# Kernel tuning notes

Measured on AMD Instinct MI355X. Metric: run time of the kernel, lower is better.

Reference implementation:

```python
import jax, jax.numpy as jnp
import numpy as np

B, M, D = 8, 4096, 512   # batch, seq_len, dim
E, P, H = 64, 1, 2048    # num_experts, slots_per_expert, expert hidden (4*dim)


def _l2norm(v, axis):
    # matches torch.nn.functional.normalize(p=2, eps=1e-12)
    n = jnp.linalg.norm(v, axis=axis, keepdims=True)
    return v / jnp.maximum(n, 1e-12)


def setup_inputs() -> dict:
    key = jax.random.key(0)
    ks = jax.random.split(key, 5)
    return {
        "x": jax.random.normal(ks[0], (B, M, D), dtype=jnp.float32),
        # phi init: normal(0, 1/sqrt(dim)) as in the module
        "phi": jax.random.normal(ks[1], (D, E, P), dtype=jnp.float32) * (1.0 / np.sqrt(D)),
        "scale": jnp.ones((1,), dtype=jnp.float32),
        # stacked expert MLP params (dim -> 4*dim -> dim, exact GELU)
        "w1": jax.random.normal(ks[2], (E, D, H), dtype=jnp.float32) * (1.0 / np.sqrt(D)),
        "b1": jnp.zeros((E, H), dtype=jnp.float32),
        "w2": jax.random.normal(ks[3], (E, H, D), dtype=jnp.float32) * (1.0 / np.sqrt(H)),
        "b2": jnp.zeros((E, D), dtype=jnp.float32),
    }


def reference(x, phi, scale, w1, b1, w2, b2):
    # Soft-MoE (algorithm 1, arXiv:2308.00951) with normalize=True
    xn = _l2norm(x, -1)                       # [B, M, D]
    phin = scale * _l2norm(phi, 0)            # [D, E, P]
    logits = jnp.einsum('bmd,dnp->bmnp', xn, phin)           # [B, M, E, P]
    d = jax.nn.softmax(logits, axis=1)                        # softmax over tokens m
    b_, m_, e_, p_ = logits.shape
    c = jax.nn.softmax(logits.reshape(b_, m_, e_ * p_), axis=-1).reshape(b_, m_, e_, p_)  # softmax over (n, p)
    xs = jnp.einsum('bmd,bmnp->bnpd', xn, d)                  # dispatch: [B, E, P, D]
    # per-expert MLP applied as grouped GEMM over expert axis n
    h = jax.nn.gelu(jnp.einsum('bnpd,ndh->bnph', xs, w1) + b1[None, :, None, :],
                    approximate=False)
    ys = jnp.einsum('bnph,nhd->bnpd', h, w2) + b2[None, :, None, :]  # [B, E, P, D]
    y = jnp.einsum('bnpd,bmnp->bmd', ys, c)                   # combine: [B, M, D]
    return y
```

## Files before the change

kernel.cpp:

```cpp
#include <hip/hip_runtime.h>
#include <hip/hip_bf16.h>
#include <math.h>


namespace {
constexpr int B = 8, M = 4096, D = 512, E = 64, H = 2048;
constexpr int NSD = 32;
constexpr int NK2 = 16;

constexpr size_t OFF_PHT  = 0;
constexpr size_t OFF_XNB  = OFF_PHT  + (size_t)D * E / 2;
constexpr size_t OFF_LOGB = OFF_XNB  + (size_t)B * M * D / 2;
constexpr size_t OFF_PMAX = OFF_LOGB + (size_t)B * M * E / 2;
constexpr size_t OFF_PSUM = OFF_PMAX + (size_t)B * NSD * E;
constexpr size_t OFF_XSP  = OFF_PSUM + (size_t)B * NSD * E;
constexpr size_t OFF_XSF  = OFF_XSP  + (size_t)NSD * B * E * D / 2;
constexpr size_t OFF_YSP  = OFF_XSF  + (size_t)E * D * B;
constexpr size_t OFF_YST  = OFF_YSP  + (size_t)NK2 * E * D * B / 2;
constexpr size_t WS_FLOATS = OFF_YST + (size_t)B * D * E / 2;
}

typedef __attribute__((ext_vector_type(8))) short short8v;
typedef __attribute__((ext_vector_type(4))) float f32x4;

static __device__ inline unsigned short f2bf(float f) {
  __hip_bfloat16 h = __float2bfloat16(f);
  return *reinterpret_cast<unsigned short*>(&h);
}
static __device__ inline float bf2f(unsigned short u) {
  unsigned int x = ((unsigned int)u) << 16;
  return __uint_as_float(x);
}
static __device__ inline short8v ld4w(const unsigned int* p, int a) {
  union { unsigned int u[4]; short8v v; } x;
  x.u[0] = p[a]; x.u[1] = p[a + 1]; x.u[2] = p[a + 2]; x.u[3] = p[a + 3];
  return x.v;
}

__global__ __launch_bounds__(256) void k_phinorm(const float* __restrict__ phi,
                                                 const float* __restrict__ scale,
                                                 unsigned short* __restrict__ phT) {
  int e = blockIdx.x;
  int t = threadIdx.x;
  float v0 = phi[(size_t)t * E + e];
  float v1 = phi[(size_t)(t + 256) * E + e];
  __shared__ float red[256];
  red[t] = v0 * v0 + v1 * v1;
  __syncthreads();
  for (int s = 128; s; s >>= 1) {
    if (t < s) red[t] += red[t + s];
    __syncthreads();
  }
  float inv = scale[0] / fmaxf(sqrtf(red[0]), 1e-12f);
  phT[(size_t)e * D + t]       = f2bf(v0 * inv);
  phT[(size_t)e * D + t + 256] = f2bf(v1 * inv);
}

__global__ __launch_bounds__(256) void k_logdis(const float* __restrict__ x,
                                                const unsigned short* __restrict__ phT,
                                                unsigned short* __restrict__ xnb,
                                                unsigned short* __restrict__ logitsb,
                                                float* __restrict__ pmax,
                                                float* __restrict__ psum,
                                                unsigned short* __restrict__ xs_part) {
  __shared__ __align__(16) unsigned char pool[80896];
  unsigned short* phs = (unsigned short*)pool;
  unsigned short* xA  = (unsigned short*)(pool + 66560);
  unsigned int* weT = (unsigned int*)pool;
  unsigned int* xnT = (unsigned int*)(pool + 16640);
  unsigned short* rp = (unsigned short*)(pool + 49920);
  __shared__ float invs[128];
  __shared__ float smax[4][64];
  __shared__ float bmax[64];
  int t = threadIdx.x;
  int lane = t & 63, w = t >> 6;
  int blk = blockIdx.x;
  int b = blk >> 5, ms = blk & 31;
  int rowbase = blk * 128;
  {
    int e = t >> 2, q0 = (t & 3) * 16;
#pragma unroll
    for (int q = 0; q < 16; q++)
      *(short8v*)&phs[e * 520 + (q0 + q) * 8] =
          *(const short8v*)&phT[(size_t)e * D + (q0 + q) * 8];
  }
  int srow = t >> 1;
  int kb = (t & 1) * 16;
  float ss = 0.f;
  f32x4 acc[2][4];
#pragma unroll
  for (int i = 0; i < 2; i++)
#pragma unroll
    for (int j = 0; j < 4; j++) acc[i][j] = (f32x4)(0.f);
  int kg = lane >> 4;
  int l15 = lane & 15;
  for (int ks = 0; ks < 16; ks++) {
    __syncthreads();
    const float4* xp = (const float4*)(x + (size_t)(rowbase + srow) * D + ks * 32 + kb);
#pragma unroll
    for (int q = 0; q < 4; q++) {
      float4 v = xp[q];
      ss += v.x * v.x + v.y * v.y + v.z * v.z + v.w * v.w;
      ushort4 u;
      u.x = f2bf(v.x); u.y = f2bf(v.y); u.z = f2bf(v.z); u.w = f2bf(v.w);
      *(ushort4*)&xA[srow * 56 + kb + q * 4] = u;
    }
    __syncthreads();
    {
      uint4 x0 = *(uint4*)&xA[srow * 56 + kb];
      uint4 x1 = *(uint4*)&xA[srow * 56 + kb + 8];
      size_t go = (size_t)(rowbase + srow) * D + ks * 32 + kb;
      *(uint4*)&xnb[go]     = x0;
      *(uint4*)&xnb[go + 8] = x1;
    }
    short8v a0 = *(short8v*)&xA[(w * 32 + l15) * 56 + kg * 8];
    short8v a1 = *(short8v*)&xA[(w * 32 + 16 + l15) * 56 + kg * 8];
    short8v b0 = *(short8v*)&phs[(l15)      * 520 + ks * 32 + kg * 8];
    short8v b1 = *(short8v*)&phs[(16 + l15) * 520 + ks * 32 + kg * 8];
    short8v b2 = *(short8v*)&phs[(32 + l15) * 520 + ks * 32 + kg * 8];
    short8v b3 = *(short8v*)&phs[(48 + l15) * 520 + ks * 32 + kg * 8];
    acc[0][0] = __builtin_amdgcn_mfma_f32_16x16x32_bf16(a0, b0, acc[0][0], 0, 0, 0);
    acc[0][1] = __builtin_amdgcn_mfma_f32_16x16x32_bf16(a0, b1, acc[0][1], 0, 0, 0);
    acc[0][2] = __builtin_amdgcn_mfma_f32_16x16x32_bf16(a0, b2, acc[0][2], 0, 0, 0);
    acc[0][3] = __builtin_amdgcn_mfma_f32_16x16x32_bf16(a0, b3, acc[0][3], 0, 0, 0);
    acc[1][0] = __builtin_amdgcn_mfma_f32_16x16x32_bf16(a1, b0, acc[1][0], 0, 0, 0);
    acc[1][1] = __builtin_amdgcn_mfma_f32_16x16x32_bf16(a1, b1, acc[1][1], 0, 0, 0);
    acc[1][2] = __builtin_amdgcn_mfma_f32_16x16x32_bf16(a1, b2, acc[1][2], 0, 0, 0);
    acc[1][3] = __builtin_amdgcn_mfma_f32_16x16x32_bf16(a1, b3, acc[1][3], 0, 0, 0);
  }
  ss += __shfl_xor(ss, 1, 64);
  float iv = 1.0f / fmaxf(sqrtf(ss), 1e-12f);
  if ((t & 1) == 0) invs[srow] = iv;
  __syncthreads();
  int rsub = kg * 4;
  float lm[4] = {-1e30f, -1e30f, -1e30f, -1e30f};
#pragma unroll
  for (int fi = 0; fi < 2; fi++)
#pragma unroll
    for (int r = 0; r < 4; r++) {
      int row = w * 32 + fi * 16 + rsub + r;
      float ivr = invs[row];
#pragma unroll
      for (int eg = 0; eg < 4; eg++) {
        float v = acc[fi][eg][r] * ivr;
        logitsb[(size_t)(rowbase + row) * E + eg * 16 + l15] = f2bf(v);
        lm[eg] = fmaxf(lm[eg], v);
      }
    }
#pragma unroll
  for (int eg = 0; eg < 4; eg++) {
    lm[eg] = fmaxf(lm[eg], __shfl_xor(lm[eg], 16, 64));
    lm[eg] = fmaxf(lm[eg], __shfl_xor(lm[eg], 32, 64));
  }
  if (lane < 16)
#pragma unroll
    for (int eg = 0; eg < 4; eg++) smax[w][eg * 16 + lane] = lm[eg];
  __syncthreads();
  if (t < 64)
    bmax[t] = fmaxf(fmaxf(smax[0][t], smax[1][t]), fmaxf(smax[2][t], smax[3][t]));
  __syncthreads();
  float ps[4] = {0.f, 0.f, 0.f, 0.f};
#pragma unroll
  for (int fi = 0; fi < 2; fi++)
#pragma unroll
    for (int r2 = 0; r2 < 2; r2++) {
      int rowA = w * 32 + fi * 16 + rsub + 2 * r2;
      float iv0 = invs[rowA], iv1 = invs[rowA + 1];
#pragma unroll
      for (int eg = 0; eg < 4; eg++) {
        float bm = bmax[eg * 16 + l15];
        float p0 = __expf(acc[fi][eg][2 * r2]     * iv0 - bm);
        float p1 = __expf(acc[fi][eg][2 * r2 + 1] * iv1 - bm);
        ps[eg] += p0 + p1;
        weT[(eg * 16 + l15) * 65 + (w * 16 + fi * 8 + (rsub >> 1) + r2)] =
            (unsigned int)f2bf(p0 * iv0) | ((unsigned int)f2bf(p1 * iv1) << 16);
      }
    }
#pragma unroll
  for (int eg = 0; eg < 4; eg++) {
    ps[eg] += __shfl_xor(ps[eg], 16, 64);
    ps[eg] += __shfl_xor(ps[eg], 32, 64);
  }
  __syncthreads();
  if (lane < 16)
#pragma unroll
    for (int eg = 0; eg < 4; eg++) smax[w][eg * 16 + lane] = ps[eg];
  __syncthreads();
  if (t < 64) {
    pmax[(size_t)blk * 64 + t] = bmax[t];
    psum[(size_t)blk * 64 + t] =
        smax[0][t] + smax[1][t] + smax[2][t] + smax[3][t];
  }
  unsigned short* outp = xs_part + ((size_t)ms * B + b) * E * D;
  for (int dc = 0; dc < 4; dc++) {
    __syncthreads();
#pragma unroll
    for (int i = 0; i < 16; i++) {
      int flat = i * 256 + t;
      int mp = flat >> 6, d2 = flat & 63;
      size_t rbase = (size_t)(rowbase + 2 * mp) * D + dc * 128 + d2 * 2;
      unsigned int ua = *(const unsigned int*)&xnb[rbase];
      unsigned int ub = *(const unsigned int*)&xnb[rbase + D];
      xnT[(2 * d2 + 0) * 65 + mp] = (ua & 0xffffu) | ((ub & 0xffffu) << 16);
      xnT[(2 * d2 + 1) * 65 + mp] = (ua >> 16) | (ub & 0xffff0000u);
    }
    __syncthreads();
    f32x4 ac3[4][2];
#pragma unroll
    for (int i = 0; i < 4; i++) { ac3[i][0] = (f32x4)(0.f); ac3[i][1] = (f32x4)(0.f); }
#pragma unroll
    for (int ks2 = 0; ks2 < 4; ks2++) {
      short8v afr[4];
#pragma unroll
      for (int et = 0; et < 4; et++)
        afr[et] = ld4w(weT, (et * 16 + l15) * 65 + ks2 * 16 + kg * 4);
#pragma unroll
      for (int dtl = 0; dtl < 2; dtl++) {
        short8v bfr = ld4w(xnT, (w * 32 + dtl * 16 + l15) * 65 + ks2 * 16 + kg * 4);
#pragma unroll
        for (int et = 0; et < 4; et++)
          ac3[et][dtl] = __builtin_amdgcn_mfma_f32_16x16x32_bf16(afr[et], bfr, ac3[et][dtl], 0, 0, 0);
      }
    }
#pragma unroll
    for (int et = 0; et < 4; et++)
#pragma unroll
      for (int dtl = 0; dtl < 2; dtl++)
#pragma unroll
        for (int r = 0; r < 4; r++) {
          int e = et * 16 + rsub + r;
          int d = w * 32 + dtl * 16 + l15;
          rp[e * 136 + d] = f2bf(ac3[et][dtl][r]);
        }
    __syncthreads();
    {
      int g = t >> 4, dch = t & 15;
#pragma unroll
      for (int pp = 0; pp < 4; pp++) {
        int el = pp * 16 + g;
        uint4 v = *(uint4*)&rp[el * 136 + dch * 8];
        *(uint4*)(outp + (size_t)el * D + dc * 128 + dch * 8) = v;
      }
    }
  }
}

__global__ __launch_bounds__(256) void k_xsred(const unsigned short* __restrict__ xs_part,
                                               const float* __restrict__ pmax,
                                               const float* __restrict__ psum,
                                               float* __restrict__ xs_f) {
  int blk = blockIdx.x;
  int b = blk >> 6, e = blk & 63;
  int t = threadIdx.x;
  float gm = -1e30f;
  for (int s = 0; s < NSD; s++)
    gm = fmaxf(gm, pmax[((size_t)(b * NSD + s)) * 64 + e]);
  float gs = 0.f;
  for (int s = 0; s < NSD; s++)
    gs += psum[((size_t)(b * NSD + s)) * 64 + e] *
          __expf(pmax[((size_t)(b * NSD + s)) * 64 + e] - gm);
  float inv = 1.0f / gs;
  size_t base = (((size_t)b * E + e) * D) / 2 + t;
  size_t slab = ((size_t)B * E * D) / 2;
  float a0 = 0.f, a1 = 0.f;
  const unsigned int* pp = (const unsigned int*)xs_part;
  for (int s = 0; s < NSD; s++) {
    float f = __expf(pmax[((size_t)(b * NSD + s)) * 64 + e] - gm);
    unsigned int v = pp[(size_t)s * slab + base];
    a0 += f * bf2f((unsigned short)(v & 0xffff));
    a1 += f * bf2f((unsigned short)(v >> 16));
  }
  int d = t * 2;
  xs_f[((size_t)e * D + d) * B + b]     = a0 * inv;
  xs_f[((size_t)e * D + d + 1) * B + b] = a1 * inv;
}

__global__ __launch_bounds__(256) void k_mlp(const float* __restrict__ w1,
                                             const float* __restrict__ b1,
                                             const float* __restrict__ w2,
                                             const float* __restrict__ xs_f,
                                             unsigned short* __restrict__ ys_part) {
  __shared__ float xsm[512 * 8];
  __shared__ float rbuf[4224];
  __shared__ float hsm[128 * 8];
  int blk = blockIdx.x;
  int e = blk >> 4, s = blk & 15;
  int t = threadIdx.x;
  const float4* xsrc = (const float4*)(xs_f + (size_t)e * D * B);
#pragma unroll
  for (int k = 0; k < 4; k++) ((float4*)xsm)[t + 256 * k] = xsrc[t + 256 * k];
  __syncthreads();
  int oct = t >> 5, jt = t & 31;
  int j0 = s * 128 + jt * 4;
  {
    const float* wp = w1 + ((size_t)e * D + oct * 64) * H + j0;
    const float* xb = xsm + oct * 64 * 8;
    float acc[4][8];
#pragma unroll
    for (int i = 0; i < 4; i++)
#pragma unroll
      for (int j = 0; j < 8; j++) acc[i][j] = 0.f;
#pragma unroll 8
    for (int d = 0; d < 64; d++) {
      float4 w = *(const float4*)(wp + (size_t)d * H);
      float x8[8];
      *(float4*)&x8[0] = *(float4*)&xb[d * 8];
      *(float4*)&x8[4] = *(float4*)&xb[d * 8 + 4];
#pragma unroll
      for (int bb = 0; bb < 8; bb++) {
        acc[0][bb] += w.x * x8[bb]; acc[1][bb] += w.y * x8[bb];
        acc[2][bb] += w.z * x8[bb]; acc[3][bb] += w.w * x8[bb];
      }
    }
    if (oct >= 4) {
      float* rb = &rbuf[((oct - 4) * 32 + jt) * 33];
#pragma unroll
      for (int i = 0; i < 4; i++) {
        *(float4*)(rb + i * 8)     = *(float4*)&acc[i][0];
        *(float4*)(rb + i * 8 + 4) = *(float4*)&acc[i][4];
      }
    }
    __syncthreads();
    if (oct < 4) {
      const float* rb = &rbuf[(oct * 32 + jt) * 33];
#pragma unroll
      for (int i = 0; i < 4; i++)
#pragma unroll
        for (int j = 0; j < 8; j++) acc[i][j] += rb[i * 8 + j];
    }
    __syncthreads();
    if (oct == 2 || oct == 3) {
      float* rb = &rbuf[((oct - 2) * 32 + jt) * 33];
#pragma unroll
      for (int i = 0; i < 4; i++) {
        *(float4*)(rb + i * 8)     = *(float4*)&acc[i][0];
        *(float4*)(rb + i * 8 + 4) = *(float4*)&acc[i][4];
      }
    }
    __syncthreads();
    if (oct < 2) {
      const float* rb = &rbuf[(oct * 32 + jt) * 33];
#pragma unroll
      for (int i = 0; i < 4; i++)
#pragma unroll
        for (int j = 0; j < 8; j++) acc[i][j] += rb[i * 8 + j];
    }
    __syncthreads();
    if (oct == 1) {
      float* rb = &rbuf[jt * 33];
#pragma unroll
      for (int i = 0; i < 4; i++) {
        *(float4*)(rb + i * 8)     = *(float4*)&acc[i][0];
        *(float4*)(rb + i * 8 + 4) = *(float4*)&acc[i][4];
      }
    }
    __syncthreads();
    if (oct == 0) {
      const float* rb = &rbuf[jt * 33];
      float4 bi = *(const float4*)(b1 + (size_t)e * H + j0);
      float bv[4] = {bi.x, bi.y, bi.z, bi.w};
#pragma unroll
      for (int i = 0; i < 4; i++)
#pragma unroll
        for (int j = 0; j < 8; j++) {
          float v = acc[i][j] + rb[i * 8 + j] + bv[i];
          hsm[(jt * 4 + i) * 8 + j] = 0.5f * v * (1.0f + erff(v * 0.70710678118654752f));
        }
    }
  }
  __syncthreads();
  {
    int kk = t >> 7, dq = t & 127;
    int d0 = dq * 4;
    const float* wp = w2 + ((size_t)e * H + s * 128 + kk * 64) * D + d0;
    const float* hb = hsm + kk * 64 * 8;
    float acc[4][8];
#pragma unroll
    for (int i = 0; i < 4; i++)
#pragma unroll
      for (int j = 0; j < 8; j++) acc[i][j] = 0.f;
#pragma unroll 8
    for (int k = 0; k < 64; k++) {
      float4 w = *(const float4*)(wp + (size_t)k * D);
      float h8[8];
      *(float4*)&h8[0] = *(float4*)&hb[k * 8];
      *(float4*)&h8[4] = *(float4*)&hb[k * 8 + 4];
#pragma unroll
      for (int bb = 0; bb < 8; bb++) {
        acc[0][bb] += w.x * h8[bb]; acc[1][bb] += w.y * h8[bb];
        acc[2][bb] += w.z * h8[bb]; acc[3][bb] += w.w * h8[bb];
      }
    }
    if (kk) {
#pragma unroll
      for (int i = 0; i < 4; i++) {
        *(float4*)&rbuf[dq * 32 + i * 8]     = *(float4*)&acc[i][0];
        *(float4*)&rbuf[dq * 32 + i * 8 + 4] = *(float4*)&acc[i][4];
      }
    }
    __syncthreads();
    if (!kk) {
      unsigned short* op = ys_part + (((size_t)s * E + e) * D + d0) * B;
#pragma unroll
      for (int i = 0; i < 4; i++) {
        unsigned short us[8];
#pragma unroll
        for (int j = 0; j < 8; j++)
          us[j] = f2bf(acc[i][j] + rbuf[dq * 32 + i * 8 + j]);
        *(uint4*)(op + (size_t)i * 8) = *(uint4*)us;
      }
    }
  }
}

__global__ __launch_bounds__(256) void k_ysred(const unsigned short* __restrict__ ys_part,
                                               const float* __restrict__ b2,
                                               unsigned short* __restrict__ ysT) {
  int e = blockIdx.x >> 2, kq = blockIdx.x & 3;
  int t = threadIdx.x;
  int i4 = kq * 256 + t;
  float a[4] = {0.f, 0.f, 0.f, 0.f};
  for (int ks = 0; ks < NK2; ks++) {
    const unsigned short* q = ys_part + ((size_t)ks * E + e) * D * B;
    ushort4 v = *(const ushort4*)(q + (size_t)i4 * 4);
    a[0] += bf2f(v.x); a[1] += bf2f(v.y); a[2] += bf2f(v.z); a[3] += bf2f(v.w);
  }
  int d = i4 >> 1, bh = (i4 & 1) * 4;
  float bias = b2[e * D + d];
#pragma unroll
  for (int j = 0; j < 4; j++)
    ysT[((size_t)(bh + j) * D + d) * E + e] = f2bf(a[j] + bias);
}

__global__ __launch_bounds__(256) void k_combine(const unsigned short* __restrict__ logitsb,
                                                 const unsigned short* __restrict__ ysT,
                                                 float* __restrict__ y) {
  __shared__ unsigned int yss[256 * 34];
  __shared__ unsigned int cb[64 * 34];
  __shared__ float red[64][4];
  __shared__ float gmx[64], gsm[64];
  int t = threadIdx.x;
  int lane = t & 63, w = t >> 6;
  int blk = blockIdx.x;
  int dg = blk & 1, mb = (blk >> 1) & 63, b = blk >> 7;
  int m0 = mb * 64;
  {
    int dloc = t >> 3, ch = t & 7;
    const unsigned short* src = ysT + ((size_t)b * D + dg * 256) * E;
#pragma unroll
    for (int p = 0; p < 8; p++) {
      int d = p * 32 + dloc;
      const unsigned int* sp = (const unsigned int*)&src[(size_t)d * E + ch * 8];
      unsigned int* dst = &yss[d * 34 + ch * 4];
      dst[0] = sp[0]; dst[1] = sp[1]; dst[2] = sp[2]; dst[3] = sp[3];
    }
  }
  int row = t >> 2, sub = t & 3;
  float r16[16];
  {
    const unsigned short* Lr = logitsb + ((size_t)(b * M + m0 + row)) * E + sub * 16;
    short8v l0 = *(const short8v*)Lr;
    short8v l1 = *(const short8v*)(Lr + 8);
#pragma unroll
    for (int k = 0; k < 8; k++) {
      r16[k]     = bf2f((unsigned short)l0[k]);
      r16[8 + k] = bf2f((unsigned short)l1[k]);
    }
  }
  float lm = -1e30f;
#pragma unroll
  for (int k = 0; k < 16; k++) lm = fmaxf(lm, r16[k]);
  red[row][sub] = lm;
  __syncthreads();
  if (sub == 0)
    gmx[row] = fmaxf(fmaxf(red[row][0], red[row][1]), fmaxf(red[row][2], red[row][3]));
  __syncthreads();
  float g = gmx[row];
  float ls = 0.f;
#pragma unroll
  for (int k = 0; k < 16; k++) {
    r16[k] = __expf(r16[k] - g);
    ls += r16[k];
  }
  red[row][sub] = ls;
  __syncthreads();
  if (sub == 0)
    gsm[row] = 1.0f / (red[row][0] + red[row][1] + red[row][2] + red[row][3]);
  __syncthreads();
  float is = gsm[row];
  {
    unsigned int us[8];
#pragma unroll
    for (int k = 0; k < 8; k++)
      us[k] = (unsigned int)f2bf(r16[2 * k] * is) |
              ((unsigned int)f2bf(r16[2 * k + 1] * is) << 16);
    unsigned int* dst = &cb[row * 34 + sub * 8];
#pragma unroll
    for (int k = 0; k < 8; k++) dst[k] = us[k];
  }
  __syncthreads();
  int kg = lane >> 4, l15 = lane & 15;
  f32x4 acc[4][4];
#pragma unroll
  for (int i = 0; i < 4; i++)
#pragma unroll
    for (int j = 0; j < 4; j++) acc[i][j] = (f32x4)(0.f);
#pragma unroll
  for (int ks = 0; ks < 2; ks++) {
    short8v afr[4];
#pragma unroll
    for (int mt = 0; mt < 4; mt++)
      afr[mt] = ld4w(cb, (mt * 16 + l15) * 34 + ks * 16 + kg * 4);
#pragma unroll
    for (int dt = 0; dt < 4; dt++) {
      short8v bfr = ld4w(yss, (w * 64 + dt * 16 + l15) * 34 + ks * 16 + kg * 4);
#pragma unroll
      for (int mt = 0; mt < 4; mt++)
        acc[mt][dt] = __builtin_amdgcn_mfma_f32_16x16x32_bf16(afr[mt], bfr, acc[mt][dt], 0, 0, 0);
    }
  }
#pragma unroll
  for (int mt = 0; mt < 4; mt++)
#pragma unroll
    for (int dt = 0; dt < 4; dt++)
#pragma unroll
      for (int r = 0; r < 4; r++) {
        int m = mt * 16 + kg * 4 + r;
        int d = dg * 256 + w * 64 + dt * 16 + l15;
        y[((size_t)(b * M + m0 + m)) * D + d] = acc[mt][dt][r];
      }
}

extern "C" void kernel_launch(void* const* d_in, const int* in_sizes, int n_in,
                              void* d_out, int out_size, void* d_ws, size_t ws_size,
                              hipStream_t stream) {
  const float* x     = (const float*)d_in[0];
  const float* phi   = (const float*)d_in[1];
  const float* scale = (const float*)d_in[2];
  const float* w1    = (const float*)d_in[3];
  const float* b1    = (const float*)d_in[4];
  const float* w2    = (const float*)d_in[5];
  const float* b2    = (const float*)d_in[6];
  float* y = (float*)d_out;
  float* ws = (float*)d_ws;
  (void)in_sizes; (void)n_in; (void)out_size; (void)ws_size;

  unsigned short* phT     = (unsigned short*)(ws + OFF_PHT);
  unsigned short* xnb     = (unsigned short*)(ws + OFF_XNB);
  unsigned short* logitsb = (unsigned short*)(ws + OFF_LOGB);
  float* pmax    = ws + OFF_PMAX;
  float* psum    = ws + OFF_PSUM;
  unsigned short* xs_part = (unsigned short*)(ws + OFF_XSP);
  float* xs_f    = ws + OFF_XSF;
  unsigned short* ys_part = (unsigned short*)(ws + OFF_YSP);
  unsigned short* ysT     = (unsigned short*)(ws + OFF_YST);

  k_phinorm<<<E, 256, 0, stream>>>(phi, scale, phT);
  k_logdis<<<B * NSD, 256, 0, stream>>>(x, phT, xnb, logitsb, pmax, psum, xs_part);
  k_xsred<<<B * E, 256, 0, stream>>>(xs_part, pmax, psum, xs_f);
  k_mlp<<<E * 16, 256, 0, stream>>>(w1, b1, w2, xs_f, ys_part);
  k_ysred<<<E * 4, 256, 0, stream>>>(ys_part, b2, ysT);
  k_combine<<<B * 64 * 2, 256, 0, stream>>>(logitsb, ysT, y);
}
```

Measured before the change: 198.7 us.

## Software-pipeline weight loads in expert MLP and flatten cross-warp reduction

The expert MLP kernel now double-buffers its fp32 weight loads, prefetching the next eight rows into registers while the current eight are multiplied, so more global loads are in flight. The previous log-depth tree reduction across the eight warp groups, with five barriers, is replaced by one shared-memory dump and a flat 8-way sum in which every thread also applies the bias and GELU. Shared memory is merged into one aliased pool and launch bounds ask for four blocks per CU. The extra prefetch registers may cause spills or reduce occupancy.

```diff
diff --git a/kernel.cpp b/kernel.cpp
--- a/kernel.cpp
+++ b/kernel.cpp
@@ -275,14 +275,16 @@
   xs_f[((size_t)e * D + d + 1) * B + b] = a1 * inv;
 }
 
-__global__ __launch_bounds__(256) void k_mlp(const float* __restrict__ w1,
-                                             const float* __restrict__ b1,
-                                             const float* __restrict__ w2,
-                                             const float* __restrict__ xs_f,
-                                             unsigned short* __restrict__ ys_part) {
-  __shared__ float xsm[512 * 8];
-  __shared__ float rbuf[4224];
-  __shared__ float hsm[128 * 8];
+__global__ __launch_bounds__(256, 4) void k_mlp(const float* __restrict__ w1,
+                                                const float* __restrict__ b1,
+                                                const float* __restrict__ w2,
+                                                const float* __restrict__ xs_f,
+                                                unsigned short* __restrict__ ys_part) {
+  __shared__ __align__(16) float pool[9472];
+  float* xsm   = pool;
+  float* rbuf1 = pool;
+  float* cbuf  = pool;
+  float* hsm   = pool + 8448;
   int blk = blockIdx.x;
   int e = blk >> 4, s = blk & 15;
   int t = threadIdx.x;
@@ -292,123 +294,130 @@
   __syncthreads();
   int oct = t >> 5, jt = t & 31;
   int j0 = s * 128 + jt * 4;
+  float acc[4][8];
+#pragma unroll
+  for (int i = 0; i < 4; i++)
+#pragma unroll
+    for (int j = 0; j < 8; j++) acc[i][j] = 0.f;
   {
     const float* wp = w1 + ((size_t)e * D + oct * 64) * H + j0;
     const float* xb = xsm + oct * 64 * 8;
-    float acc[4][8];
-#pragma unroll
-    for (int i = 0; i < 4; i++)
-#pragma unroll
-      for (int j = 0; j < 8; j++) acc[i][j] = 0.f;
-#pragma unroll 8
-    for (int d = 0; d < 64; d++) {
-      float4 w = *(const float4*)(wp + (size_t)d * H);
-      float x8[8];
-      *(float4*)&x8[0] = *(float4*)&xb[d * 8];
-      *(float4*)&x8[4] = *(float4*)&xb[d * 8 + 4];
-#pragma unroll
-      for (int bb = 0; bb < 8; bb++) {
-        acc[0][bb] += w.x * x8[bb]; acc[1][bb] += w.y * x8[bb];
-        acc[2][bb] += w.z * x8[bb]; acc[3][bb] += w.w * x8[bb];
-      }
-    }
-    if (oct >= 4) {
-      float* rb = &rbuf[((oct - 4) * 32 + jt) * 33];
-#pragma unroll
-      for (int i = 0; i < 4; i++) {
-        *(float4*)(rb + i * 8)     = *(float4*)&acc[i][0];
-        *(float4*)(rb + i * 8 + 4) = *(float4*)&acc[i][4];
-      }
-    }
-    __syncthreads();
-    if (oct < 4) {
-      const float* rb = &rbuf[(oct * 32 + jt) * 33];
-#pragma unroll
-      for (int i = 0; i < 4; i++)
-#pragma unroll
-        for (int j = 0; j < 8; j++) acc[i][j] += rb[i * 8 + j];
-    }
-    __syncthreads();
-    if (oct == 2 || oct == 3) {
-      float* rb = &rbuf[((oct - 2) * 32 + jt) * 33];
-#pragma unroll
-      for (int i = 0; i < 4; i++) {
-        *(float4*)(rb + i * 8)     = *(float4*)&acc[i][0];
-        *(float4*)(rb + i * 8 + 4) = *(float4*)&acc[i][4];
-      }
-    }
-    __syncthreads();
-    if (oct < 2) {
-      const float* rb = &rbuf[(oct * 32 + jt) * 33];
-#pragma unroll
-      for (int i = 0; i < 4; i++)
-#pragma unroll
-        for (int j = 0; j < 8; j++) acc[i][j] += rb[i * 8 + j];
-    }
-    __syncthreads();
-    if (oct == 1) {
-      float* rb = &rbuf[jt * 33];
-#pragma unroll
-      for (int i = 0; i < 4; i++) {
-        *(float4*)(rb + i * 8)     = *(float4*)&acc[i][0];
-        *(float4*)(rb + i * 8 + 4) = *(float4*)&acc[i][4];
-      }
-    }
-    __syncthreads();
-    if (oct == 0) {
-      const float* rb = &rbuf[jt * 33];
-      float4 bi = *(const float4*)(b1 + (size_t)e * H + j0);
-      float bv[4] = {bi.x, bi.y, bi.z, bi.w};
-#pragma unroll
-      for (int i = 0; i < 4; i++)
-#pragma unroll
-        for (int j = 0; j < 8; j++) {
-          float v = acc[i][j] + rb[i * 8 + j] + bv[i];
-          hsm[(jt * 4 + i) * 8 + j] = 0.5f * v * (1.0f + erff(v * 0.70710678118654752f));
+    float4 wb[8];
+#pragma unroll
+    for (int p = 0; p < 8; p++) wb[p] = *(const float4*)(wp + (size_t)p * H);
+#pragma unroll
+    for (int dblk = 0; dblk < 64; dblk += 8) {
+      float4 wn[8];
+      if (dblk < 56) {
+#pragma unroll
+        for (int p = 0; p < 8; p++)
+          wn[p] = *(const float4*)(wp + (size_t)(dblk + 8 + p) * H);
+      }
+#pragma unroll
+      for (int p = 0; p < 8; p++) {
+        float x8[8];
+        *(float4*)&x8[0] = *(float4*)&xb[(dblk + p) * 8];
+        *(float4*)&x8[4] = *(float4*)&xb[(dblk + p) * 8 + 4];
+        float4 w = wb[p];
+#pragma unroll
+        for (int bb = 0; bb < 8; bb++) {
+          acc[0][bb] += w.x * x8[bb]; acc[1][bb] += w.y * x8[bb];
+          acc[2][bb] += w.z * x8[bb]; acc[3][bb] += w.w * x8[bb];
         }
-    }
-  }
-  __syncthreads();
-  {
-    int kk = t >> 7, dq = t & 127;
-    int d0 = dq * 4;
+      }
+      if (dblk < 56) {
+#pragma unroll
+        for (int p = 0; p < 8; p++) wb[p] = wn[p];
+      }
+    }
+  }
+  __syncthreads();
+  {
+    float* rb = rbuf1 + ((size_t)oct * 32 + jt) * 33;
+#pragma unroll
+    for (int i = 0; i < 4; i++) {
+      *(float4*)(rb + i * 8)     = *(float4*)&acc[i][0];
+      *(float4*)(rb + i * 8 + 4) = *(float4*)&acc[i][4];
+    }
+  }
+  __syncthreads();
+  {
+    int j = t >> 1, b0 = (t & 1) * 4;
+    float a0 = 0.f, a1 = 0.f, a2 = 0.f, a3 = 0.f;
+#pragma unroll
+    for (int o = 0; o < 8; o++) {
+      const float* rv = rbuf1 + o * 1056 + (j >> 2) * 33 + (j & 3) * 8 + b0;
+      float4 v = *(const float4*)rv;
+      a0 += v.x; a1 += v.y; a2 += v.z; a3 += v.w;
+    }
+    float bias = b1[(size_t)e * H + s * 128 + j];
+    a0 += bias; a1 += bias; a2 += bias; a3 += bias;
+    float4 o4;
+    o4.x = 0.5f * a0 * (1.0f + erff(a0 * 0.70710678118654752f));
+    o4.y = 0.5f * a1 * (1.0f + erff(a1 * 0.70710678118654752f));
+    o4.z = 0.5f * a2 * (1.0f + erff(a2 * 0.70710678118654752f));
+    o4.w = 0.5f * a3 * (1.0f + erff(a3 * 0.70710678118654752f));
+    *(float4*)&hsm[j * 8 + b0] = o4;
+  }
+  __syncthreads();
+  int kk = t >> 7, dq = t & 127;
+  int d0 = dq * 4;
+  float ac2[4][8];
+#pragma unroll
+  for (int i = 0; i < 4; i++)
+#pragma unroll
+    for (int j = 0; j < 8; j++) ac2[i][j] = 0.f;
+  {
     const float* wp = w2 + ((size_t)e * H + s * 128 + kk * 64) * D + d0;
     const float* hb = hsm + kk * 64 * 8;
-    float acc[4][8];
-#pragma unroll
-    for (int i = 0; i < 4; i++)
-#pragma unroll
-      for (int j = 0; j < 8; j++) acc[i][j] = 0.f;
-#pragma unroll 8
-    for (int k = 0; k < 64; k++) {
-      float4 w = *(const float4*)(wp + (size_t)k * D);
-      float h8[8];
-      *(float4*)&h8[0] = *(float4*)&hb[k * 8];
-      *(float4*)&h8[4] = *(float4*)&hb[k * 8 + 4];
-#pragma unroll
-      for (int bb = 0; bb < 8; bb++) {
-        acc[0][bb] += w.x * h8[bb]; acc[1][bb] += w.y * h8[bb];
-        acc[2][bb] += w.z * h8[bb]; acc[3][bb] += w.w * h8[bb];
-      }
-    }
-    if (kk) {
-#pragma unroll
-      for (int i = 0; i < 4; i++) {
-        *(float4*)&rbuf[dq * 32 + i * 8]     = *(float4*)&acc[i][0];
-        *(float4*)&rbuf[dq * 32 + i * 8 + 4] = *(float4*)&acc[i][4];
-      }
-    }
-    __syncthreads();
-    if (!kk) {
-      unsigned short* op = ys_part + (((size_t)s * E + e) * D + d0) * B;
-#pragma unroll
-      for (int i = 0; i < 4; i++) {
-        unsigned short us[8];
-#pragma unroll
-        for (int j = 0; j < 8; j++)
-          us[j] = f2bf(acc[i][j] + rbuf[dq * 32 + i * 8 + j]);
-        *(uint4*)(op + (size_t)i * 8) = *(uint4*)us;
-      }
+    float4 wb[8];
+#pragma unroll
+    for (int p = 0; p < 8; p++) wb[p] = *(const float4*)(wp + (size_t)p * D);
+#pragma unroll
+    for (int kblk = 0; kblk < 64; kblk += 8) {
+      float4 wn[8];
+      if (kblk < 56) {
+#pragma unroll
+        for (int p = 0; p < 8; p++)
+          wn[p] = *(const float4*)(wp + (size_t)(kblk + 8 + p) * D);
+      }
+#pragma unroll
+      for (int p = 0; p < 8; p++) {
+        float h8[8];
+        *(float4*)&h8[0] = *(float4*)&hb[(kblk + p) * 8];
+        *(float4*)&h8[4] = *(float4*)&hb[(kblk + p) * 8 + 4];
+        float4 w = wb[p];
+#pragma unroll
+        for (int bb = 0; bb < 8; bb++) {
+          ac2[0][bb] += w.x * h8[bb]; ac2[1][bb] += w.y * h8[bb];
+          ac2[2][bb] += w.z * h8[bb]; ac2[3][bb] += w.w * h8[bb];
+        }
+      }
+      if (kblk < 56) {
+#pragma unroll
+        for (int p = 0; p < 8; p++) wb[p] = wn[p];
+      }
+    }
+  }
+  if (kk) {
+    float* cb = cbuf + dq * 33;
+#pragma unroll
+    for (int i = 0; i < 4; i++) {
+      *(float4*)(cb + i * 8)     = *(float4*)&ac2[i][0];
+      *(float4*)(cb + i * 8 + 4) = *(float4*)&ac2[i][4];
+    }
+  }
+  __syncthreads();
+  if (!kk) {
+    const float* cb = cbuf + dq * 33;
+    unsigned short* op = ys_part + (((size_t)s * E + e) * D + d0) * B;
+#pragma unroll
+    for (int i = 0; i < 4; i++) {
+      unsigned short us[8];
+#pragma unroll
+      for (int j = 0; j < 8; j++)
+        us[j] = f2bf(ac2[i][j] + cb[i * 8 + j]);
+      *(uint4*)(op + (size_t)i * 8) = *(uint4*)us;
     }
   }
 }
```

New measurement: 224.3 us. 12.9% more time.

## Split expert MLP into split-K first GEMM and separate second GEMM kernel

Applied to the files above, without the earlier changes.

The fused per-expert MLP kernel is replaced by two kernels. The first computes partial W1 products over 32-row D slices with 2048 blocks, writing bf16 partials into reused workspace. The second reduces those partials, applies bias and GELU, and runs the W2 GEMM with 32 K-splits. This removes the in-block shared-memory tree reduction and its barriers, and raises block count to feed more CUs on the weight-bandwidth-bound GEMMs. The cost is an extra launch, extra partial-sum traffic, and bf16 rounding of the pre-activation partials.

```diff
diff --git a/kernel.cpp b/kernel.cpp
--- a/kernel.cpp
+++ b/kernel.cpp
@@ -6,7 +6,8 @@
 namespace {
 constexpr int B = 8, M = 4096, D = 512, E = 64, H = 2048;
 constexpr int NSD = 32;
-constexpr int NK2 = 16;
+constexpr int NH1 = 16;
+constexpr int NK2 = 32;
 
 constexpr size_t OFF_PHT  = 0;
 constexpr size_t OFF_XNB  = OFF_PHT  + (size_t)D * E / 2;
@@ -15,8 +16,7 @@
 constexpr size_t OFF_PSUM = OFF_PMAX + (size_t)B * NSD * E;
 constexpr size_t OFF_XSP  = OFF_PSUM + (size_t)B * NSD * E;
 constexpr size_t OFF_XSF  = OFF_XSP  + (size_t)NSD * B * E * D / 2;
-constexpr size_t OFF_YSP  = OFF_XSF  + (size_t)E * D * B;
-constexpr size_t OFF_YST  = OFF_YSP  + (size_t)NK2 * E * D * B / 2;
+constexpr size_t OFF_YST  = OFF_XSF  + (size_t)E * D * B;
 constexpr size_t WS_FLOATS = OFF_YST + (size_t)B * D * E / 2;
 }
 
@@ -275,141 +275,99 @@
   xs_f[((size_t)e * D + d + 1) * B + b] = a1 * inv;
 }
 
-__global__ __launch_bounds__(256) void k_mlp(const float* __restrict__ w1,
-                                             const float* __restrict__ b1,
-                                             const float* __restrict__ w2,
+__global__ __launch_bounds__(256) void k_g1h(const float* __restrict__ w1,
                                              const float* __restrict__ xs_f,
-                                             unsigned short* __restrict__ ys_part) {
-  __shared__ float xsm[512 * 8];
-  __shared__ float rbuf[4224];
-  __shared__ float hsm[128 * 8];
+                                             unsigned short* __restrict__ h_part) {
+  __shared__ float xsm[32 * 8];
   int blk = blockIdx.x;
-  int e = blk >> 4, s = blk & 15;
-  int t = threadIdx.x;
-  const float4* xsrc = (const float4*)(xs_f + (size_t)e * D * B);
-#pragma unroll
-  for (int k = 0; k < 4; k++) ((float4*)xsm)[t + 256 * k] = xsrc[t + 256 * k];
-  __syncthreads();
-  int oct = t >> 5, jt = t & 31;
-  int j0 = s * 128 + jt * 4;
+  int js = blk & 1, ds = (blk >> 1) & 15, e = blk >> 5;
+  int t = threadIdx.x;
+  if (t < 64)
+    ((float4*)xsm)[t] = ((const float4*)(xs_f + ((size_t)e * D + ds * 32) * B))[t];
+  __syncthreads();
+  int j0 = js * 1024 + t * 4;
+  const float* wp = w1 + ((size_t)e * D + ds * 32) * H + j0;
+  float acc[4][8];
+#pragma unroll
+  for (int i = 0; i < 4; i++)
+#pragma unroll
+    for (int j = 0; j < 8; j++) acc[i][j] = 0.f;
+#pragma unroll 8
+  for (int d = 0; d < 32; d++) {
+    float4 w = *(const float4*)(wp + (size_t)d * H);
+    float x8[8];
+    *(float4*)&x8[0] = *(float4*)&xsm[d * 8];
+    *(float4*)&x8[4] = *(float4*)&xsm[d * 8 + 4];
+#pragma unroll
+    for (int bb = 0; bb < 8; bb++) {
+      acc[0][bb] += w.x * x8[bb]; acc[1][bb] += w.y * x8[bb];
+      acc[2][bb] += w.z * x8[bb]; acc[3][bb] += w.w * x8[bb];
+    }
+  }
+  unsigned short* op = h_part + (((size_t)ds * E + e) * H + j0) * B;
+#pragma unroll
+  for (int i = 0; i < 4; i++) {
+    unsigned short us[8];
+#pragma unroll
+    for (int j = 0; j < 8; j++) us[j] = f2bf(acc[i][j]);
+    *(uint4*)(op + (size_t)i * 8) = *(uint4*)us;
+  }
+}
+
+__global__ __launch_bounds__(256) void k_g2(const float* __restrict__ w2,
+                                            const float* __restrict__ b1,
+                                            const unsigned short* __restrict__ h_part,
+                                            unsigned short* __restrict__ ys_part) {
+  __shared__ float hsm[64 * 8];
+  int blk = blockIdx.x;
+  int ks = blk & 31, e = blk >> 5;
+  int t = threadIdx.x;
   {
-    const float* wp = w1 + ((size_t)e * D + oct * 64) * H + j0;
-    const float* xb = xsm + oct * 64 * 8;
-    float acc[4][8];
-#pragma unroll
-    for (int i = 0; i < 4; i++)
-#pragma unroll
-      for (int j = 0; j < 8; j++) acc[i][j] = 0.f;
+    int k = t >> 2, bq = (t & 3) * 2;
+    int j = ks * 64 + k;
+    const unsigned short* base = h_part + ((size_t)e * H + j) * B + bq;
+    float a0 = 0.f, a1 = 0.f;
+#pragma unroll
+    for (int sl = 0; sl < NH1; sl++) {
+      unsigned int v = *(const unsigned int*)(base + (size_t)sl * E * H * B);
+      a0 += bf2f((unsigned short)(v & 0xffff));
+      a1 += bf2f((unsigned short)(v >> 16));
+    }
+    float bias = b1[(size_t)e * H + j];
+    a0 += bias; a1 += bias;
+    hsm[k * 8 + bq]     = 0.5f * a0 * (1.0f + erff(a0 * 0.70710678118654752f));
+    hsm[k * 8 + bq + 1] = 0.5f * a1 * (1.0f + erff(a1 * 0.70710678118654752f));
+  }
+  __syncthreads();
+  int d0 = t * 2;
+  const float* wp = w2 + ((size_t)e * H + ks * 64) * D + d0;
+  float acc[2][8];
+#pragma unroll
+  for (int i = 0; i < 2; i++)
+#pragma unroll
+    for (int j = 0; j < 8; j++) acc[i][j] = 0.f;
 #pragma unroll 8
-    for (int d = 0; d < 64; d++) {
-      float4 w = *(const float4*)(wp + (size_t)d * H);
-      float x8[8];
-      *(float4*)&x8[0] = *(float4*)&xb[d * 8];
-      *(float4*)&x8[4] = *(float4*)&xb[d * 8 + 4];
-#pragma unroll
-      for (int bb = 0; bb < 8; bb++) {
-        acc[0][bb] += w.x * x8[bb]; acc[1][bb] += w.y * x8[bb];
-        acc[2][bb] += w.z * x8[bb]; acc[3][bb] += w.w * x8[bb];
-      }
-    }
-    if (oct >= 4) {
-      float* rb = &rbuf[((oct - 4) * 32 + jt) * 33];
-#pragma unroll
-      for (int i = 0; i < 4; i++) {
-        *(float4*)(rb + i * 8)     = *(float4*)&acc[i][0];
-        *(float4*)(rb + i * 8 + 4) = *(float4*)&acc[i][4];
-      }
-    }
-    __syncthreads();
-    if (oct < 4) {
-      const float* rb = &rbuf[(oct * 32 + jt) * 33];
-#pragma unroll
-      for (int i = 0; i < 4; i++)
-#pragma unroll
-        for (int j = 0; j < 8; j++) acc[i][j] += rb[i * 8 + j];
-    }
-    __syncthreads();
-    if (oct == 2 || oct == 3) {
-      float* rb = &rbuf[((oct - 2) * 32 + jt) * 33];
-#pragma unroll
-      for (int i = 0; i < 4; i++) {
-        *(float4*)(rb + i * 8)     = *(float4*)&acc[i][0];
-        *(float4*)(rb + i * 8 + 4) = *(float4*)&acc[i][4];
-      }
-    }
-    __syncthreads();
-    if (oct < 2) {
-      const float* rb = &rbuf[(oct * 32 + jt) * 33];
-#pragma unroll
-      for (int i = 0; i < 4; i++)
-#pragma unroll
-        for (int j = 0; j < 8; j++) acc[i][j] += rb[i * 8 + j];
-    }
-    __syncthreads();
-    if (oct == 1) {
-      float* rb = &rbuf[jt * 33];
-#pragma unroll
-      for (int i = 0; i < 4; i++) {
-        *(float4*)(rb + i * 8)     = *(float4*)&acc[i][0];
-        *(float4*)(rb + i * 8 + 4) = *(float4*)&acc[i][4];
-      }
-    }
-    __syncthreads();
-    if (oct == 0) {
-      const float* rb = &rbuf[jt * 33];
-      float4 bi = *(const float4*)(b1 + (size_t)e * H + j0);
-      float bv[4] = {bi.x, bi.y, bi.z, bi.w};
-#pragma unroll
-      for (int i = 0; i < 4; i++)
-#pragma unroll
-        for (int j = 0; j < 8; j++) {
-          float v = acc[i][j] + rb[i * 8 + j] + bv[i];
-          hsm[(jt * 4 + i) * 8 + j] = 0.5f * v * (1.0f + erff(v * 0.70710678118654752f));
-        }
-    }
-  }
-  __syncthreads();
+  for (int k = 0; k < 64; k++) {
+    float2 w = *(const float2*)(wp + (size_t)k * D);
+    float h8[8];
+    *(float4*)&h8[0] = *(float4*)&hsm[k * 8];
+    *(float4*)&h8[4] = *(float4*)&hsm[k * 8 + 4];
+#pragma unroll
+    for (int bb = 0; bb < 8; bb++) {
+      acc[0][bb] += w.x * h8[bb];
+      acc[1][bb] += w.y * h8[bb];
+    }
+  }
+  unsigned short* op = ys_part + (((size_t)ks * E + e) * D + d0) * B;
   {
-    int kk = t >> 7, dq = t & 127;
-    int d0 = dq * 4;
-    const float* wp = w2 + ((size_t)e * H + s * 128 + kk * 64) * D + d0;
-    const float* hb = hsm + kk * 64 * 8;
-    float acc[4][8];
-#pragma unroll
-    for (int i = 0; i < 4; i++)
-#pragma unroll
-      for (int j = 0; j < 8; j++) acc[i][j] = 0.f;
-#pragma unroll 8
-    for (int k = 0; k < 64; k++) {
-      float4 w = *(const float4*)(wp + (size_t)k * D);
-      float h8[8];
-      *(float4*)&h8[0] = *(float4*)&hb[k * 8];
-      *(float4*)&h8[4] = *(float4*)&hb[k * 8 + 4];
-#pragma unroll
-      for (int bb = 0; bb < 8; bb++) {
-        acc[0][bb] += w.x * h8[bb]; acc[1][bb] += w.y * h8[bb];
-        acc[2][bb] += w.z * h8[bb]; acc[3][bb] += w.w * h8[bb];
-      }
-    }
-    if (kk) {
-#pragma unroll
-      for (int i = 0; i < 4; i++) {
-        *(float4*)&rbuf[dq * 32 + i * 8]     = *(float4*)&acc[i][0];
-        *(float4*)&rbuf[dq * 32 + i * 8 + 4] = *(float4*)&acc[i][4];
-      }
-    }
-    __syncthreads();
-    if (!kk) {
-      unsigned short* op = ys_part + (((size_t)s * E + e) * D + d0) * B;
-#pragma unroll
-      for (int i = 0; i < 4; i++) {
-        unsigned short us[8];
-#pragma unroll
-        for (int j = 0; j < 8; j++)
-          us[j] = f2bf(acc[i][j] + rbuf[dq * 32 + i * 8 + j]);
-        *(uint4*)(op + (size_t)i * 8) = *(uint4*)us;
-      }
-    }
+    unsigned short us[16];
+#pragma unroll
+    for (int j = 0; j < 8; j++) {
+      us[j]     = f2bf(acc[0][j]);
+      us[8 + j] = f2bf(acc[1][j]);
+    }
+    *(uint4*)(op)     = *(uint4*)&us[0];
+    *(uint4*)(op + 8) = *(uint4*)&us[8];
   }
 }
 
@@ -552,13 +510,15 @@
   float* psum    = ws + OFF_PSUM;
   unsigned short* xs_part = (unsigned short*)(ws + OFF_XSP);
   float* xs_f    = ws + OFF_XSF;
-  unsigned short* ys_part = (unsigned short*)(ws + OFF_YSP);
   unsigned short* ysT     = (unsigned short*)(ws + OFF_YST);
+  unsigned short* h_part  = xnb;
+  unsigned short* ys_part = xs_part;
 
   k_phinorm<<<E, 256, 0, stream>>>(phi, scale, phT);
   k_logdis<<<B * NSD, 256, 0, stream>>>(x, phT, xnb, logitsb, pmax, psum, xs_part);
   k_xsred<<<B * E, 256, 0, stream>>>(xs_part, pmax, psum, xs_f);
-  k_mlp<<<E * 16, 256, 0, stream>>>(w1, b1, w2, xs_f, ys_part);
+  k_g1h<<<E * NH1 * 2, 256, 0, stream>>>(w1, xs_f, h_part);
+  k_g2<<<E * NK2, 256, 0, stream>>>(w2, b1, h_part, ys_part);
   k_ysred<<<E * 4, 256, 0, stream>>>(ys_part, b2, ysT);
   k_combine<<<B * 64 * 2, 256, 0, stream>>>(logitsb, ysT, y);
 }
```

New measurement: 208.6 us. +5.0%, slower.
